# Kernel tuning notes

Measured on AMD Instinct MI355X. Metric: run time of the kernel, lower is better.

The kernel has to match this reference:

```python
import jax, jax.numpy as jnp
import numpy as np

C = 256
CQK = C // 8
EPS_NORM = 1e-12  # torch F.normalize eps
EPS_TEMP = 1e-6


def _xavier(key, shape):
    fan_out, fan_in = shape
    limit = float(np.sqrt(6.0 / (fan_in + fan_out)))
    return jax.random.uniform(key, shape, jnp.float32, -limit, limit)


def setup_inputs() -> dict:
    key = jax.random.key(0)
    ks = jax.random.split(key, 6)
    x = jax.random.normal(ks[0], (8, C, 64, 64), jnp.float32)
    Wq = _xavier(ks[1], (CQK, C))
    Wk = _xavier(ks[2], (CQK, C))
    # value conv uses default Conv2d init (kaiming uniform); any random init is fine for a numeric baseline
    bound = float(1.0 / np.sqrt(C))
    Wv = jax.random.uniform(ks[3], (C, C), jnp.float32, -bound, bound)
    bq = jax.random.uniform(ks[4], (CQK,), jnp.float32, -bound, bound)
    bk = jax.random.uniform(ks[5], (CQK,), jnp.float32, -bound, bound)
    bv = jax.random.uniform(jax.random.fold_in(key, 7), (C,), jnp.float32, -bound, bound)
    gamma = jnp.ones((1,), jnp.float32)
    temperature = jnp.array(1.0, jnp.float32)
    return {"x": x, "Wq": Wq, "bq": bq, "Wk": Wk, "bk": bk, "Wv": Wv, "bv": bv,
            "gamma": gamma, "temperature": temperature}


def _l2norm_lastdim(t):
    # F.normalize(p=2, dim=-1): divide by max(||t||_2, eps) along last axis
    n = jnp.sqrt(jnp.sum(t * t, axis=-1, keepdims=True))
    return t / jnp.maximum(n, EPS_NORM)


def reference(x, Wq, bq, Wk, bk, Wv, bv, gamma, temperature):
    B, Cc, H, W = x.shape
    N = H * W
    xf = x.reshape(B, Cc, N)  # (B, C, N)
    # 1x1 convs == channel GEMMs
    q = jnp.einsum('oc,bcn->bon', Wq, xf) + bq[:, None]   # (B, C/8, N)
    k = jnp.einsum('oc,bcn->bon', Wk, xf) + bk[:, None]   # (B, C/8, N)
    v = jnp.einsum('oc,bcn->bon', Wv, xf) + bv[:, None]   # (B, C, N)
    # NOTE: normalization is over the SPATIAL dim (dim=-1), matching the source
    qn = _l2norm_lastdim(q)
    kn = _l2norm_lastdim(k)
    energy = jnp.einsum('bcn,bcm->bnm', qn, kn) / (temperature + EPS_TEMP)
    energy = energy + jnp.eye(N, dtype=energy.dtype)
    attention = jax.nn.softmax(energy, axis=-1)  # (B, N, N)
    # out[b,c,m] = sum_n v[b,c,n] * attention[b,m,n]
    out = jnp.einsum('bcn,bmn->bcm', v, attention)
    out = out.reshape(B, Cc, H, W)
    return gamma * out + x
```

## Files before the change

kernel.cpp:

```cpp
#include <hip/hip_runtime.h>
#include <hip/hip_bf16.h>
#include <math.h>

typedef __attribute__((ext_vector_type(8))) short short8;
typedef __attribute__((ext_vector_type(4))) float floatx4;
typedef __attribute__((ext_vector_type(16))) float floatx16;

#define B_ 8
#define C_ 256
#define N_ 4096
#define LOG2E 1.4426950408889634f
#define XSTRIDE 548

static __device__ __forceinline__ unsigned short f2bf(float f) {
  union { float f; unsigned int u; } v; v.f = f;
  unsigned int u = v.u;
  u += 0x7FFFu + ((u >> 16) & 1u);
  return (unsigned short)(u >> 16);
}
static __device__ __forceinline__ float bf2f(unsigned short h) {
  union { unsigned int u; float f; } v; v.u = ((unsigned int)h) << 16; return v.f;
}
static __device__ __forceinline__ unsigned int pk2(float a, float b) {
  return __builtin_amdgcn_perm(__float_as_uint(b), __float_as_uint(a), 0x07060302u);
}

__global__ void prep_kernel(const float* __restrict__ Wq, const float* __restrict__ Wk,
                            const float* __restrict__ Wv,
                            unsigned short* __restrict__ wqb, unsigned short* __restrict__ wkb,
                            unsigned short* __restrict__ wvb, float* __restrict__ ssq) {
  int t = blockIdx.x * 256 + threadIdx.x;
  if (t < 512) ssq[t] = 0.0f;
  if (t < 8192) { wqb[t] = f2bf(Wq[t]); wkb[t] = f2bf(Wk[t]); }
  int tv = t - 8192;
  if (tv >= 0 && tv < 65536) wvb[tv] = f2bf(Wv[tv]);
}

__launch_bounds__(512, 4)
__global__ void qkv_kernel(const float* __restrict__ x,
                           const unsigned short* __restrict__ wqb,
                           const unsigned short* __restrict__ wkb,
                           const unsigned short* __restrict__ wvb,
                           const float* __restrict__ bq, const float* __restrict__ bk,
                           const float* __restrict__ bv,
                           unsigned short* __restrict__ qbf, unsigned short* __restrict__ kbf,
                           unsigned short* __restrict__ vbf, float* __restrict__ ssq) {
  __shared__ __align__(16) char Xt[64 * XSTRIDE];
  int b = blockIdx.x & 7;
  int nblk = blockIdx.x >> 3;
  int tid = threadIdx.x;
  int w = tid >> 6, lane = tid & 63;
  int r = lane & 15, g = lane >> 4;
  int nh = w & 3, ch = w >> 2;
  int n0 = nblk * 64;

  {
    int q = tid & 15, cpw = tid >> 4;
    const float* xb = x + ((size_t)b << 20) + n0 + q * 4;
    #pragma unroll
    for (int p = 0; p < 4; ++p) {
      int cp = p * 32 + cpw;
      const float* s0 = xb + ((size_t)(2 * cp) << 12);
      float4 a  = *(const float4*)s0;
      float4 bb = *(const float4*)(s0 + 4096);
      char* dst = Xt + cp * 4;
      *(unsigned int*)(dst + (q * 4 + 0) * XSTRIDE) = pk2(a.x, bb.x);
      *(unsigned int*)(dst + (q * 4 + 1) * XSTRIDE) = pk2(a.y, bb.y);
      *(unsigned int*)(dst + (q * 4 + 2) * XSTRIDE) = pk2(a.z, bb.z);
      *(unsigned int*)(dst + (q * 4 + 3) * XSTRIDE) = pk2(a.w, bb.w);
    }
  }
  __syncthreads();

  short8 xf[8];
  #pragma unroll
  for (int ks = 0; ks < 8; ++ks) {
    const char* src = Xt + (nh * 16 + r) * XSTRIDE + (ks * 32 + g * 8) * 2;
    union { unsigned int u[4]; short8 s8; } t;
    t.u[0] = *(const unsigned int*)(src);
    t.u[1] = *(const unsigned int*)(src + 4);
    t.u[2] = *(const unsigned int*)(src + 8);
    t.u[3] = *(const unsigned int*)(src + 12);
    xf[ks] = t.s8;
  }
  int nw = n0 + nh * 16;
  floatx4 zero = {0.f, 0.f, 0.f, 0.f};
  unsigned short* vt = vbf + (size_t)b * C_ * N_;
  const unsigned short* wqk = ch ? wkb : wqb;
  const float* bias = ch ? bk : bq;
  unsigned short* qkdst = ch ? kbf : qbf;
  int sbase = ch ? 256 : 0;

  const unsigned short* vwb = wvb + (size_t)(ch * 128 + r) * 256 + g * 8;
  const unsigned short* qwb = wqk + (size_t)r * 256 + g * 8;

  short8 wf[2][4];
  #pragma unroll
  for (int j = 0; j < 4; ++j) wf[0][j] = *(const short8*)(vwb + j * 32);

  #pragma unroll
  for (int t = 0; t < 10; ++t) {
    const unsigned short* curb = (t < 8) ? (vwb + t * 4096) : (qwb + (t - 8) * 4096);
    const unsigned short* nxtb = (t < 7) ? (vwb + (t + 1) * 4096)
                                         : ((t < 9) ? (qwb + (t - 7) * 4096) : curb);
    floatx4 acc = zero;
    #pragma unroll
    for (int j = 0; j < 4; ++j) wf[1][j] = *(const short8*)(curb + (4 + j) * 32);
    #pragma unroll
    for (int j = 0; j < 4; ++j)
      acc = __builtin_amdgcn_mfma_f32_16x16x32_bf16(wf[0][j], xf[j], acc, 0, 0, 0);
    #pragma unroll
    for (int j = 0; j < 4; ++j) wf[0][j] = *(const short8*)(nxtb + j * 32);
    #pragma unroll
    for (int j = 0; j < 4; ++j)
      acc = __builtin_amdgcn_mfma_f32_16x16x32_bf16(wf[1][j], xf[4 + j], acc, 0, 0, 0);

    if (t < 8) {
      int otile = ch * 8 + t;
      #pragma unroll
      for (int rr = 0; rr < 4; ++rr) {
        int oc = otile * 16 + g * 4 + rr;
        int n = nw + r;
        vt[(size_t)(n >> 3) * 2048 + oc * 8 + (n & 7)] = f2bf(acc[rr] + bv[oc]);
      }
    } else {
      #pragma unroll
      for (int rr = 0; rr < 4; ++rr) {
        int oc = (t - 8) * 16 + g * 4 + rr;
        float val = acc[rr] + bias[oc];
        qkdst[(size_t)(b * N_ + nw + r) * 32 + oc] = f2bf(val);
        float s = val * val;
        s += __shfl_xor(s, 1);
        s += __shfl_xor(s, 2);
        s += __shfl_xor(s, 4);
        s += __shfl_xor(s, 8);
        if (r == 0) atomicAdd(&ssq[sbase + b * 32 + oc], s);
      }
    }
  }
}

__launch_bounds__(256, 2)
__global__ void attn_kernel(const unsigned short* __restrict__ qbf,
                            const unsigned short* __restrict__ kbf,
                            const unsigned short* __restrict__ vbf,
                            const float* __restrict__ ssq, const float* __restrict__ temp,
                            const float* __restrict__ x, const float* __restrict__ gamma,
                            float* __restrict__ out) {
  int b = blockIdx.x & 7, mblk = blockIdx.x >> 3;
  int tid = threadIdx.x;
  int w = tid >> 6, lane = tid & 63, c = lane & 31, h = lane >> 5;
  int ms = w & 1, cvh = w >> 1;
  const unsigned short* qb = qbf + (size_t)b * N_ * 32;
  const unsigned short* kb = kbf + (size_t)b * N_ * 32;
  const unsigned short* vt = vbf + (size_t)b * C_ * N_;
  int mrow = mblk * 64 + ms * 32 + c;
  int tdiag = mblk * 2 + ms;

  float invt = LOG2E / (temp[0] + 1e-6f);
  short8 q0r = *(const short8*)&qb[mrow * 32 + h * 8];
  short8 q1r = *(const short8*)&qb[mrow * 32 + 16 + h * 8];
  short8 qf0, qf1;
  #pragma unroll
  for (int j = 0; j < 8; ++j) {
    int ch0 = h * 8 + j, ch1 = 16 + h * 8 + j;
    float s0 = invt * rsqrtf(fmaxf(ssq[b * 32 + ch0] * ssq[256 + b * 32 + ch0], 1e-24f));
    float s1 = invt * rsqrtf(fmaxf(ssq[b * 32 + ch1] * ssq[256 + b * 32 + ch1], 1e-24f));
    ((unsigned short*)&qf0)[j] = f2bf(bf2f(((const unsigned short*)&q0r)[j]) * s0);
    ((unsigned short*)&qf1)[j] = f2bf(bf2f(((const unsigned short*)&q1r)[j]) * s1);
  }

  const unsigned short* kp = kb + (size_t)c * 32 + h * 8;
  const unsigned short* vp0 = vt + h * 2048 + (cvh * 128 + c) * 8;
  const unsigned short* vp1 = vp0 + 4096;

  floatx16 minit;
  #pragma unroll
  for (int i = 0; i < 16; ++i) minit[i] = -2.0f * LOG2E;
  floatx16 zero16 = {0,0,0,0,0,0,0,0,0,0,0,0,0,0,0,0};
  floatx16 acc[4] = {zero16, zero16, zero16, zero16};
  float Lp = 0.0f;
  short8 kfA[2], kfB[2], afA[8], afB[8];

  kfA[0] = *(const short8*)kp;
  kfA[1] = *(const short8*)(kp + 16);
  kp += 1024;
  #pragma unroll
  for (int k = 0; k < 8; ++k)
    afA[k] = *(const short8*)(((k >> 2) ? vp1 : vp0) + (k & 3) * 256);
  vp0 += 8192; vp1 += 8192;

  auto body = [&](int t, short8 (&kfC)[2], short8 (&kfN)[2],
                  short8 (&afC)[8], short8 (&afN)[8]) {
    if (t + 1 < 128) {
      kfN[0] = *(const short8*)kp;
      kfN[1] = *(const short8*)(kp + 16);
      kp += 1024;
      #pragma unroll
      for (int k = 0; k < 8; ++k)
        afN[k] = *(const short8*)(((k >> 2) ? vp1 : vp0) + (k & 3) * 256);
      vp0 += 8192; vp1 += 8192;
    }
    floatx16 s = __builtin_amdgcn_mfma_f32_32x32x16_bf16(kfC[0], qf0, minit, 0, 0, 0);
    s = __builtin_amdgcn_mfma_f32_32x32x16_bf16(kfC[1], qf1, s, 0, 0, 0);
    if (t == tdiag && ((c >> 2) & 1) == h)
      s[(c & 3) | ((c >> 3) << 2)] += LOG2E;
    float p[16];
    float ls = 0.0f;
    #pragma unroll
    for (int i = 0; i < 16; ++i) {
      p[i] = __builtin_amdgcn_exp2f(s[i]);
      ls += p[i];
    }
    Lp += ls;
    #pragma unroll
    for (int t16 = 0; t16 < 2; ++t16) {
      unsigned int q0 = pk2(p[8*t16+0], p[8*t16+1]);
      unsigned int q1 = pk2(p[8*t16+2], p[8*t16+3]);
      unsigned int q2 = pk2(p[8*t16+4], p[8*t16+5]);
      unsigned int q3 = pk2(p[8*t16+6], p[8*t16+7]);
      asm volatile("v_permlane32_swap_b32 %0, %1" : "+v"(q2), "+v"(q0));
      asm volatile("v_permlane32_swap_b32 %0, %1" : "+v"(q3), "+v"(q1));
      union { unsigned int u[4]; short8 s8; } bf;
      bf.u[0] = q0; bf.u[1] = q1; bf.u[2] = q2; bf.u[3] = q3;
      #pragma unroll
      for (int cvt = 0; cvt < 4; ++cvt)
        acc[cvt] = __builtin_amdgcn_mfma_f32_32x32x16_bf16(afC[t16 * 4 + cvt], bf.s8, acc[cvt], 0, 0, 0);
    }
  };

  #pragma unroll 1
  for (int t = 0; t < 128; t += 2) {
    body(t, kfA, kfB, afA, afB);
    body(t + 1, kfB, kfA, afB, afA);
  }

  Lp += __shfl_xor(Lp, 32);
  float linv = 1.0f / Lp;
  float gam = gamma[0];
  #pragma unroll
  for (int cvt = 0; cvt < 4; ++cvt)
    #pragma unroll
    for (int i = 0; i < 16; ++i) {
      int cv = cvh * 128 + cvt * 32 + (i & 3) + 8 * (i >> 2) + 4 * h;
      size_t idx = ((size_t)(b * C_ + cv) << 12) + mrow;
      out[idx] = gam * acc[cvt][i] * linv + x[idx];
    }
}

extern "C" void kernel_launch(void* const* d_in, const int* in_sizes, int n_in,
                              void* d_out, int out_size, void* d_ws, size_t ws_size,
                              hipStream_t stream) {
  (void)in_sizes; (void)n_in; (void)out_size; (void)ws_size;
  const float* x    = (const float*)d_in[0];
  const float* Wq   = (const float*)d_in[1];
  const float* bq   = (const float*)d_in[2];
  const float* Wk   = (const float*)d_in[3];
  const float* bk   = (const float*)d_in[4];
  const float* Wv   = (const float*)d_in[5];
  const float* bv   = (const float*)d_in[6];
  const float* gam  = (const float*)d_in[7];
  const float* temp = (const float*)d_in[8];
  float* out = (float*)d_out;

  char* ws = (char*)d_ws;
  unsigned short* vbf = (unsigned short*)ws;
  unsigned short* qbf = (unsigned short*)(ws + (16u << 20));
  unsigned short* kbf = (unsigned short*)(ws + (18u << 20));
  unsigned short* wqb = (unsigned short*)(ws + (20u << 20));
  unsigned short* wkb = wqb + 8192;
  unsigned short* wvb = wkb + 8192;
  float* ssq = (float*)(wvb + 65536);

  prep_kernel<<<dim3(288), dim3(256), 0, stream>>>(Wq, Wk, Wv, wqb, wkb, wvb, ssq);
  qkv_kernel<<<dim3(512), dim3(512), 0, stream>>>(x, wqb, wkb, wvb, bq, bk, bv, qbf, kbf, vbf, ssq);
  attn_kernel<<<dim3(512), dim3(256), 0, stream>>>(qbf, kbf, vbf, ssq, temp, x, gam, out);
}
```

Measured before the change: 181.4 us.

## Compute two query tiles per wave to reuse K/V fragment loads

Each wave now handles two 32-row query tiles instead of one, so every K and V fragment loaded from global memory feeds twice as many MFMAs. The block covers 128 query rows and the grid is halved to 256 blocks. Launch bounds drop to one block per SM to allow the doubled accumulator register footprint. The cost is lower occupancy and fewer blocks than the MI355X's 256 CUs can absorb evenly, which may reduce latency hiding.

```diff
diff --git a/kernel.cpp b/kernel.cpp
--- a/kernel.cpp
+++ b/kernel.cpp
@@ -140,7 +140,7 @@
   }
 }
 
-__launch_bounds__(256, 2)
+__launch_bounds__(256, 1)
 __global__ void attn_kernel(const unsigned short* __restrict__ qbf,
                             const unsigned short* __restrict__ kbf,
                             const unsigned short* __restrict__ vbf,
@@ -150,24 +150,32 @@
   int b = blockIdx.x & 7, mblk = blockIdx.x >> 3;
   int tid = threadIdx.x;
   int w = tid >> 6, lane = tid & 63, c = lane & 31, h = lane >> 5;
-  int ms = w & 1, cvh = w >> 1;
+  int ms = w >> 1, cvh = w & 1;
   const unsigned short* qb = qbf + (size_t)b * N_ * 32;
   const unsigned short* kb = kbf + (size_t)b * N_ * 32;
   const unsigned short* vt = vbf + (size_t)b * C_ * N_;
-  int mrow = mblk * 64 + ms * 32 + c;
-  int tdiag = mblk * 2 + ms;
+  int mrow0 = mblk * 128 + ms * 64 + c;
+  int tdiag0 = mblk * 4 + ms * 2;
 
   float invt = LOG2E / (temp[0] + 1e-6f);
-  short8 q0r = *(const short8*)&qb[mrow * 32 + h * 8];
-  short8 q1r = *(const short8*)&qb[mrow * 32 + 16 + h * 8];
-  short8 qf0, qf1;
+  float qsc[16];
   #pragma unroll
   for (int j = 0; j < 8; ++j) {
     int ch0 = h * 8 + j, ch1 = 16 + h * 8 + j;
-    float s0 = invt * rsqrtf(fmaxf(ssq[b * 32 + ch0] * ssq[256 + b * 32 + ch0], 1e-24f));
-    float s1 = invt * rsqrtf(fmaxf(ssq[b * 32 + ch1] * ssq[256 + b * 32 + ch1], 1e-24f));
-    ((unsigned short*)&qf0)[j] = f2bf(bf2f(((const unsigned short*)&q0r)[j]) * s0);
-    ((unsigned short*)&qf1)[j] = f2bf(bf2f(((const unsigned short*)&q1r)[j]) * s1);
+    qsc[j]     = invt * rsqrtf(fmaxf(ssq[b * 32 + ch0] * ssq[256 + b * 32 + ch0], 1e-24f));
+    qsc[8 + j] = invt * rsqrtf(fmaxf(ssq[b * 32 + ch1] * ssq[256 + b * 32 + ch1], 1e-24f));
+  }
+  short8 qf[2][2];
+  #pragma unroll
+  for (int mt = 0; mt < 2; ++mt) {
+    int mr = mrow0 + mt * 32;
+    short8 a = *(const short8*)&qb[mr * 32 + h * 8];
+    short8 bq8 = *(const short8*)&qb[mr * 32 + 16 + h * 8];
+    #pragma unroll
+    for (int j = 0; j < 8; ++j) {
+      ((unsigned short*)&qf[mt][0])[j] = f2bf(bf2f(((const unsigned short*)&a)[j]) * qsc[j]);
+      ((unsigned short*)&qf[mt][1])[j] = f2bf(bf2f(((const unsigned short*)&bq8)[j]) * qsc[8 + j]);
+    }
   }
 
   const unsigned short* kp = kb + (size_t)c * 32 + h * 8;
@@ -178,8 +186,12 @@
   #pragma unroll
   for (int i = 0; i < 16; ++i) minit[i] = -2.0f * LOG2E;
   floatx16 zero16 = {0,0,0,0,0,0,0,0,0,0,0,0,0,0,0,0};
-  floatx16 acc[4] = {zero16, zero16, zero16, zero16};
-  float Lp = 0.0f;
+  floatx16 acc[2][4];
+  #pragma unroll
+  for (int mt = 0; mt < 2; ++mt)
+    #pragma unroll
+    for (int cvt = 0; cvt < 4; ++cvt) acc[mt][cvt] = zero16;
+  float Lp0 = 0.0f, Lp1 = 0.0f;
   short8 kfA[2], kfB[2], afA[8], afB[8];
 
   kfA[0] = *(const short8*)kp;
@@ -201,31 +213,34 @@
         afN[k] = *(const short8*)(((k >> 2) ? vp1 : vp0) + (k & 3) * 256);
       vp0 += 8192; vp1 += 8192;
     }
-    floatx16 s = __builtin_amdgcn_mfma_f32_32x32x16_bf16(kfC[0], qf0, minit, 0, 0, 0);
-    s = __builtin_amdgcn_mfma_f32_32x32x16_bf16(kfC[1], qf1, s, 0, 0, 0);
-    if (t == tdiag && ((c >> 2) & 1) == h)
-      s[(c & 3) | ((c >> 3) << 2)] += LOG2E;
-    float p[16];
-    float ls = 0.0f;
-    #pragma unroll
-    for (int i = 0; i < 16; ++i) {
-      p[i] = __builtin_amdgcn_exp2f(s[i]);
-      ls += p[i];
-    }
-    Lp += ls;
-    #pragma unroll
-    for (int t16 = 0; t16 < 2; ++t16) {
-      unsigned int q0 = pk2(p[8*t16+0], p[8*t16+1]);
-      unsigned int q1 = pk2(p[8*t16+2], p[8*t16+3]);
-      unsigned int q2 = pk2(p[8*t16+4], p[8*t16+5]);
-      unsigned int q3 = pk2(p[8*t16+6], p[8*t16+7]);
-      asm volatile("v_permlane32_swap_b32 %0, %1" : "+v"(q2), "+v"(q0));
-      asm volatile("v_permlane32_swap_b32 %0, %1" : "+v"(q3), "+v"(q1));
-      union { unsigned int u[4]; short8 s8; } bf;
-      bf.u[0] = q0; bf.u[1] = q1; bf.u[2] = q2; bf.u[3] = q3;
-      #pragma unroll
-      for (int cvt = 0; cvt < 4; ++cvt)
-        acc[cvt] = __builtin_amdgcn_mfma_f32_32x32x16_bf16(afC[t16 * 4 + cvt], bf.s8, acc[cvt], 0, 0, 0);
+    #pragma unroll
+    for (int mt = 0; mt < 2; ++mt) {
+      floatx16 s = __builtin_amdgcn_mfma_f32_32x32x16_bf16(kfC[0], qf[mt][0], minit, 0, 0, 0);
+      s = __builtin_amdgcn_mfma_f32_32x32x16_bf16(kfC[1], qf[mt][1], s, 0, 0, 0);
+      if (t == tdiag0 + mt && ((c >> 2) & 1) == h)
+        s[(c & 3) | ((c >> 3) << 2)] += LOG2E;
+      float p[16];
+      float ls = 0.0f;
+      #pragma unroll
+      for (int i = 0; i < 16; ++i) {
+        p[i] = __builtin_amdgcn_exp2f(s[i]);
+        ls += p[i];
+      }
+      if (mt == 0) Lp0 += ls; else Lp1 += ls;
+      #pragma unroll
+      for (int t16 = 0; t16 < 2; ++t16) {
+        unsigned int q0 = pk2(p[8*t16+0], p[8*t16+1]);
+        unsigned int q1 = pk2(p[8*t16+2], p[8*t16+3]);
+        unsigned int q2 = pk2(p[8*t16+4], p[8*t16+5]);
+        unsigned int q3 = pk2(p[8*t16+6], p[8*t16+7]);
+        asm volatile("v_permlane32_swap_b32 %0, %1" : "+v"(q2), "+v"(q0));
+        asm volatile("v_permlane32_swap_b32 %0, %1" : "+v"(q3), "+v"(q1));
+        union { unsigned int u[4]; short8 s8; } bf;
+        bf.u[0] = q0; bf.u[1] = q1; bf.u[2] = q2; bf.u[3] = q3;
+        #pragma unroll
+        for (int cvt = 0; cvt < 4; ++cvt)
+          acc[mt][cvt] = __builtin_amdgcn_mfma_f32_32x32x16_bf16(afC[t16 * 4 + cvt], bf.s8, acc[mt][cvt], 0, 0, 0);
+      }
     }
   };
 
@@ -235,17 +250,20 @@
     body(t + 1, kfB, kfA, afB, afA);
   }
 
-  Lp += __shfl_xor(Lp, 32);
-  float linv = 1.0f / Lp;
+  Lp0 += __shfl_xor(Lp0, 32);
+  Lp1 += __shfl_xor(Lp1, 32);
+  float linv[2] = {1.0f / Lp0, 1.0f / Lp1};
   float gam = gamma[0];
   #pragma unroll
-  for (int cvt = 0; cvt < 4; ++cvt)
-    #pragma unroll
-    for (int i = 0; i < 16; ++i) {
-      int cv = cvh * 128 + cvt * 32 + (i & 3) + 8 * (i >> 2) + 4 * h;
-      size_t idx = ((size_t)(b * C_ + cv) << 12) + mrow;
-      out[idx] = gam * acc[cvt][i] * linv + x[idx];
-    }
+  for (int mt = 0; mt < 2; ++mt)
+    #pragma unroll
+    for (int cvt = 0; cvt < 4; ++cvt)
+      #pragma unroll
+      for (int i = 0; i < 16; ++i) {
+        int cv = cvh * 128 + cvt * 32 + (i & 3) + 8 * (i >> 2) + 4 * h;
+        size_t idx = ((size_t)(b * C_ + cv) << 12) + mrow0 + mt * 32;
+        out[idx] = gam * acc[mt][cvt][i] * linv[mt] + x[idx];
+      }
 }
 
 extern "C" void kernel_launch(void* const* d_in, const int* in_sizes, int n_in,
@@ -274,5 +292,5 @@
 
   prep_kernel<<<dim3(288), dim3(256), 0, stream>>>(Wq, Wk, Wv, wqb, wkb, wvb, ssq);
   qkv_kernel<<<dim3(512), dim3(512), 0, stream>>>(x, wqb, wkb, wvb, bq, bk, bv, qbf, kbf, vbf, ssq);
-  attn_kernel<<<dim3(512), dim3(256), 0, stream>>>(qbf, kbf, vbf, ssq, temp, x, gam, out);
-}
+  attn_kernel<<<dim3(256), dim3(256), 0, stream>>>(qbf, kbf, vbf, ssq, temp, x, gam, out);
+}
```

Measured after the change: 191.6 us. 1.06x slower.

## Store V and attention probabilities in FP8 and use FP8 MFMA for PV

Applied to the files above, without the earlier changes.

The value projection is now written as FP8 in a new 32-wide interleaved layout, and the PV product converts softmax probabilities to packed FP8 and runs 32x32x16 FP8 MFMAs in place of BF16. This halves V bytes loaded in the attention inner loop and the V fragment registers, which targets memory traffic and register pressure. The row-sum reduction is also written as a tree. The cost is a large loss of precision in both V and P, which may exceed tolerance.

```diff
diff --git a/kernel.cpp b/kernel.cpp
--- a/kernel.cpp
+++ b/kernel.cpp
@@ -44,7 +44,7 @@
                            const float* __restrict__ bq, const float* __restrict__ bk,
                            const float* __restrict__ bv,
                            unsigned short* __restrict__ qbf, unsigned short* __restrict__ kbf,
-                           unsigned short* __restrict__ vbf, float* __restrict__ ssq) {
+                           unsigned char* __restrict__ vbf, float* __restrict__ ssq) {
   __shared__ __align__(16) char Xt[64 * XSTRIDE];
   int b = blockIdx.x & 7;
   int nblk = blockIdx.x >> 3;
@@ -85,7 +85,7 @@
   }
   int nw = n0 + nh * 16;
   floatx4 zero = {0.f, 0.f, 0.f, 0.f};
-  unsigned short* vt = vbf + (size_t)b * C_ * N_;
+  unsigned char* vt = vbf + (size_t)b * C_ * N_;
   const unsigned short* wqk = ch ? wkb : wqb;
   const float* bias = ch ? bk : bq;
   unsigned short* qkdst = ch ? kbf : qbf;
@@ -97,6 +97,9 @@
   short8 wf[2][4];
   #pragma unroll
   for (int j = 0; j < 4; ++j) wf[0][j] = *(const short8*)(vwb + j * 32);
+
+  int n = nw + r;
+  size_t vsb = (size_t)(n >> 5) * 8192 + ((n >> 3) & 1) * 16 + ((n >> 4) & 1) * 8 + (n & 7);
 
   #pragma unroll
   for (int t = 0; t < 10; ++t) {
@@ -120,8 +123,9 @@
       #pragma unroll
       for (int rr = 0; rr < 4; ++rr) {
         int oc = otile * 16 + g * 4 + rr;
-        int n = nw + r;
-        vt[(size_t)(n >> 3) * 2048 + oc * 8 + (n & 7)] = f2bf(acc[rr] + bv[oc]);
+        float val = acc[rr] + bv[oc];
+        int pk8 = __builtin_amdgcn_cvt_pk_fp8_f32(val, val, 0, false);
+        vt[vsb + (size_t)oc * 32] = (unsigned char)(pk8 & 0xFF);
       }
     } else {
       #pragma unroll
@@ -143,7 +147,7 @@
 __launch_bounds__(256, 2)
 __global__ void attn_kernel(const unsigned short* __restrict__ qbf,
                             const unsigned short* __restrict__ kbf,
-                            const unsigned short* __restrict__ vbf,
+                            const unsigned char* __restrict__ vbf,
                             const float* __restrict__ ssq, const float* __restrict__ temp,
                             const float* __restrict__ x, const float* __restrict__ gamma,
                             float* __restrict__ out) {
@@ -153,7 +157,7 @@
   int ms = w & 1, cvh = w >> 1;
   const unsigned short* qb = qbf + (size_t)b * N_ * 32;
   const unsigned short* kb = kbf + (size_t)b * N_ * 32;
-  const unsigned short* vt = vbf + (size_t)b * C_ * N_;
+  const unsigned char* vt = vbf + (size_t)b * C_ * N_;
   int mrow = mblk * 64 + ms * 32 + c;
   int tdiag = mblk * 2 + ms;
 
@@ -171,8 +175,7 @@
   }
 
   const unsigned short* kp = kb + (size_t)c * 32 + h * 8;
-  const unsigned short* vp0 = vt + h * 2048 + (cvh * 128 + c) * 8;
-  const unsigned short* vp1 = vp0 + 4096;
+  const unsigned char* vp = vt + (size_t)(cvh * 128 + c) * 32 + h * 16;
 
   floatx16 minit;
   #pragma unroll
@@ -180,52 +183,49 @@
   floatx16 zero16 = {0,0,0,0,0,0,0,0,0,0,0,0,0,0,0,0};
   floatx16 acc[4] = {zero16, zero16, zero16, zero16};
   float Lp = 0.0f;
-  short8 kfA[2], kfB[2], afA[8], afB[8];
+  short8 kfA[2], kfB[2], afA[4], afB[4];
 
   kfA[0] = *(const short8*)kp;
   kfA[1] = *(const short8*)(kp + 16);
   kp += 1024;
   #pragma unroll
-  for (int k = 0; k < 8; ++k)
-    afA[k] = *(const short8*)(((k >> 2) ? vp1 : vp0) + (k & 3) * 256);
-  vp0 += 8192; vp1 += 8192;
+  for (int cvt = 0; cvt < 4; ++cvt)
+    afA[cvt] = *(const short8*)(vp + cvt * 1024);
+  vp += 8192;
 
   auto body = [&](int t, short8 (&kfC)[2], short8 (&kfN)[2],
-                  short8 (&afC)[8], short8 (&afN)[8]) {
+                  short8 (&afC)[4], short8 (&afN)[4]) {
     if (t + 1 < 128) {
       kfN[0] = *(const short8*)kp;
       kfN[1] = *(const short8*)(kp + 16);
       kp += 1024;
       #pragma unroll
-      for (int k = 0; k < 8; ++k)
-        afN[k] = *(const short8*)(((k >> 2) ? vp1 : vp0) + (k & 3) * 256);
-      vp0 += 8192; vp1 += 8192;
+      for (int cvt = 0; cvt < 4; ++cvt)
+        afN[cvt] = *(const short8*)(vp + cvt * 1024);
+      vp += 8192;
     }
     floatx16 s = __builtin_amdgcn_mfma_f32_32x32x16_bf16(kfC[0], qf0, minit, 0, 0, 0);
     s = __builtin_amdgcn_mfma_f32_32x32x16_bf16(kfC[1], qf1, s, 0, 0, 0);
     if (t == tdiag && ((c >> 2) & 1) == h)
       s[(c & 3) | ((c >> 3) << 2)] += LOG2E;
     float p[16];
-    float ls = 0.0f;
-    #pragma unroll
-    for (int i = 0; i < 16; ++i) {
-      p[i] = __builtin_amdgcn_exp2f(s[i]);
-      ls += p[i];
-    }
-    Lp += ls;
+    #pragma unroll
+    for (int i = 0; i < 16; ++i) p[i] = __builtin_amdgcn_exp2f(s[i]);
+    Lp += (((p[0] + p[1]) + (p[2] + p[3])) + ((p[4] + p[5]) + (p[6] + p[7])))
+        + (((p[8] + p[9]) + (p[10] + p[11])) + ((p[12] + p[13]) + (p[14] + p[15])));
     #pragma unroll
     for (int t16 = 0; t16 < 2; ++t16) {
-      unsigned int q0 = pk2(p[8*t16+0], p[8*t16+1]);
-      unsigned int q1 = pk2(p[8*t16+2], p[8*t16+3]);
-      unsigned int q2 = pk2(p[8*t16+4], p[8*t16+5]);
-      unsigned int q3 = pk2(p[8*t16+6], p[8*t16+7]);
-      asm volatile("v_permlane32_swap_b32 %0, %1" : "+v"(q2), "+v"(q0));
-      asm volatile("v_permlane32_swap_b32 %0, %1" : "+v"(q3), "+v"(q1));
-      union { unsigned int u[4]; short8 s8; } bf;
-      bf.u[0] = q0; bf.u[1] = q1; bf.u[2] = q2; bf.u[3] = q3;
-      #pragma unroll
-      for (int cvt = 0; cvt < 4; ++cvt)
-        acc[cvt] = __builtin_amdgcn_mfma_f32_32x32x16_bf16(afC[t16 * 4 + cvt], bf.s8, acc[cvt], 0, 0, 0);
+      int d0 = __builtin_amdgcn_cvt_pk_fp8_f32(p[8*t16+0], p[8*t16+1], 0, false);
+      d0 = __builtin_amdgcn_cvt_pk_fp8_f32(p[8*t16+2], p[8*t16+3], d0, true);
+      int d1 = __builtin_amdgcn_cvt_pk_fp8_f32(p[8*t16+4], p[8*t16+5], 0, false);
+      d1 = __builtin_amdgcn_cvt_pk_fp8_f32(p[8*t16+6], p[8*t16+7], d1, true);
+      asm volatile("v_permlane32_swap_b32 %0, %1" : "+v"(d1), "+v"(d0));
+      long bl = (long)(((unsigned long long)(unsigned)d1 << 32) | (unsigned)d0);
+      #pragma unroll
+      for (int cvt = 0; cvt < 4; ++cvt) {
+        union { short8 s8; long l[2]; } u; u.s8 = afC[cvt];
+        acc[cvt] = __builtin_amdgcn_mfma_f32_32x32x16_fp8_fp8(u.l[t16], bl, acc[cvt], 0, 0, 0);
+      }
     }
   };
 
@@ -264,7 +264,7 @@
   float* out = (float*)d_out;
 
   char* ws = (char*)d_ws;
-  unsigned short* vbf = (unsigned short*)ws;
+  unsigned char* vbf  = (unsigned char*)ws;
   unsigned short* qbf = (unsigned short*)(ws + (16u << 20));
   unsigned short* kbf = (unsigned short*)(ws + (18u << 20));
   unsigned short* wqb = (unsigned short*)(ws + (20u << 20));
```

Result: faster. 158.7 us (-12.5%).
